# Performance work log

Hardware: AMD Instinct MI355X
Metric: run time of the kernel (lower is better)

Reference implementation:

```python
import jax, jax.numpy as jnp
import numpy as np

B, X, H, R, M = 256, 512, 1024, 512, 512
F_BIAS = 1.0

def setup_inputs() -> dict:
    key = jax.random.key(0)
    ks = jax.random.split(key, 8)
    s = lambda fan: 1.0 / np.sqrt(fan)
    return {
        "x": jax.random.normal(ks[0], (B, X), jnp.float32),
        "h": jax.random.normal(ks[1], (B, H), jnp.float32),
        "c": jnp.tanh(jax.random.normal(ks[2], (B, H), jnp.float32)),
        "hmem": jax.random.normal(ks[3], (B, M, R), jnp.float32),
        "W_full": jax.random.normal(ks[4], (X + R + H, R + 4 * H), jnp.float32) * s(X + R + H),
        "bias": jnp.zeros((R + 4 * H,), jnp.float32),
        "W_full1": jax.random.normal(ks[5], (X + R + H, R + H), jnp.float32) * s(X + R + H),
        "bias1": jnp.zeros((R + H,), jnp.float32),
        "trans_w": jax.random.normal(ks[6], (R, X + H), jnp.float32) * s(X + H),
        "trans_b": jnp.zeros((R,), jnp.float32),
        "fc_w": jax.random.normal(ks[7], (M, X + H), jnp.float32) * s(X + H),
        "fc_b": jnp.zeros((M,), jnp.float32),
    }

def reference(x, h, c, hmem, W_full, bias, W_full1, bias1, trans_w, trans_b, fc_w, fc_b):
    h_size = H
    # soft read head over memory slots
    read_head = jnp.concatenate([x, c], axis=1) @ fc_w.T + fc_b          # [B, M]
    h_index = jax.nn.softmax(read_head, axis=1)                          # [B, M]
    h_entry = jnp.einsum('bm,bmr->br', h_index, hmem)                    # [B, R]
    # gated double-projection
    concat = jnp.concatenate([x, c, h_entry], axis=1)                    # [B, X+H+R]
    g = jax.nn.sigmoid(concat @ W_full1 + bias1)                         # [B, R+H]
    gate = jnp.concatenate([jnp.ones_like(x), g], axis=1)                # [B, X+H+R]
    pre = (concat * gate) @ W_full + bias                                # [B, R+4H]
    i = pre[:, 0*h_size:1*h_size]
    j = pre[:, 1*h_size:2*h_size]
    f = pre[:, 2*h_size:3*h_size]
    o = pre[:, 3*h_size:4*h_size]
    om = pre[:, 4*h_size:]                                               # [B, R]
    new_c = jnp.tanh(c * jax.nn.sigmoid(f + F_BIAS) + jax.nn.sigmoid(i) * jnp.tanh(j))
    new_h = new_c * jax.nn.sigmoid(o)
    r_out = h_entry * jax.nn.sigmoid(om)
    # steady-state write: soft index (detached), broadcast overwrite
    w_index = jax.lax.stop_gradient(h_index)                             # [B, M]
    w_val = jnp.concatenate([x, new_c], axis=1) @ trans_w.T + trans_b    # [B, R]
    new_hmem = w_val[:, None, :] * w_index[:, :, None] + hmem * (1.0 - w_index[:, :, None])
    new_r = jnp.concatenate([new_h, r_out], axis=1)                      # [B, H+R]
    return new_r, new_h, new_c, new_hmem
```

## Files before the change

### kernel.cpp

```cpp
#include <hip/hip_runtime.h>
#include <hip/hip_bf16.h>
#include <cstddef>

#define BB 256
#define XX 512
#define HH 1024
#define RR 512
#define MM 512
#define KCAT 2048
#define KXC 1536
#define NFULL 4608
#define NG 1536

#define OFF_NH (BB*1536)
#define OFF_NC (OFF_NH + BB*HH)
#define OFF_HM (OFF_NC + BB*HH)

typedef __attribute__((ext_vector_type(8))) short bf16x8;
typedef __attribute__((ext_vector_type(4))) short s16x4;
typedef __attribute__((ext_vector_type(4))) float f32x4;

__device__ __forceinline__ float sigm(float x) { return 1.0f / (1.0f + expf(-x)); }

__device__ __forceinline__ unsigned short f2bf(float f) {
    unsigned u = __float_as_uint(f);
    u = u + 0x7fffu + ((u >> 16) & 1u);
    return (unsigned short)(u >> 16);
}
__device__ __forceinline__ float bf2f(unsigned short h) {
    return __uint_as_float((unsigned)h << 16);
}


__global__ __launch_bounds__(256) void convw_k(const float* __restrict__ src,
                                               short* __restrict__ hi,
                                               short* __restrict__ lo,
                                               int n8) {
    int i = blockIdx.x * 256 + threadIdx.x;
    if (i >= n8) return;
    size_t e0 = (size_t)i * 8;
    short hs[8], ls[8];
    #pragma unroll
    for (int q = 0; q < 2; ++q) {
        float4 v = reinterpret_cast<const float4*>(src + e0)[q];
        float f[4] = {v.x, v.y, v.z, v.w};
        #pragma unroll
        for (int e = 0; e < 4; ++e) {
            unsigned short hb = f2bf(f[e]);
            hs[q * 4 + e] = (short)hb;
            ls[q * 4 + e] = (short)f2bf(f[e] - bf2f(hb));
        }
    }
    *reinterpret_cast<bf16x8*>(hi + e0) = *reinterpret_cast<bf16x8*>(&hs[0]);
    *reinterpret_cast<bf16x8*>(lo + e0) = *reinterpret_cast<bf16x8*>(&ls[0]);
}

__global__ __launch_bounds__(256) void convt_k(const float* __restrict__ W,
                                               int Kdim, int Ndim,
                                               short* __restrict__ Thi,
                                               short* __restrict__ Tlo) {
    __shared__ __align__(16) short lh[64][72];
    __shared__ __align__(16) short ll[64][72];
    const int tid = threadIdx.x;
    const int k0 = blockIdx.x * 64, n0 = blockIdx.y * 64;
    {
        int kr = (tid >> 4) * 4;
        int nc = (tid & 15) * 4;
        #pragma unroll
        for (int i = 0; i < 4; ++i) {
            float4 v = *reinterpret_cast<const float4*>(W + (size_t)(k0 + kr + i) * Ndim + n0 + nc);
            float f[4] = {v.x, v.y, v.z, v.w};
            #pragma unroll
            for (int e = 0; e < 4; ++e) {
                unsigned short hb = f2bf(f[e]);
                lh[nc + e][kr + i] = (short)hb;
                ll[nc + e][kr + i] = (short)f2bf(f[e] - bf2f(hb));
            }
        }
    }
    __syncthreads();
    {
        int nl = tid >> 2;
        int kq = (tid & 3) * 16;
        size_t base = (size_t)(n0 + nl) * Kdim + k0 + kq;
        *reinterpret_cast<bf16x8*>(Thi + base)     = *reinterpret_cast<const bf16x8*>(&lh[nl][kq]);
        *reinterpret_cast<bf16x8*>(Thi + base + 8) = *reinterpret_cast<const bf16x8*>(&lh[nl][kq + 8]);
        *reinterpret_cast<bf16x8*>(Tlo + base)     = *reinterpret_cast<const bf16x8*>(&ll[nl][kq]);
        *reinterpret_cast<bf16x8*>(Tlo + base + 8) = *reinterpret_cast<const bf16x8*>(&ll[nl][kq + 8]);
    }
}

__global__ __launch_bounds__(256) void prep_k(const float* __restrict__ x,
                                              const float* __restrict__ c,
                                              short* __restrict__ cat_hi, short* __restrict__ cat_lo,
                                              short* __restrict__ gat_hi, short* __restrict__ gat_lo,
                                              short* __restrict__ xnc_hi, short* __restrict__ xnc_lo) {
    int i = blockIdx.x * 256 + threadIdx.x;
    int e0 = i * 4;
    int b = e0 / KXC, q = e0 - b * KXC;
    float4 v = (q < XX) ? *reinterpret_cast<const float4*>(x + (size_t)b * XX + q)
                        : *reinterpret_cast<const float4*>(c + (size_t)b * HH + (q - XX));
    float f[4] = {v.x, v.y, v.z, v.w};
    s16x4 hv, lv;
    #pragma unroll
    for (int e = 0; e < 4; ++e) {
        unsigned short hb = f2bf(f[e]);
        hv[e] = (short)hb;
        lv[e] = (short)f2bf(f[e] - bf2f(hb));
    }
    *reinterpret_cast<s16x4*>(cat_hi + (size_t)b * KCAT + q) = hv;
    *reinterpret_cast<s16x4*>(cat_lo + (size_t)b * KCAT + q) = lv;
    if (q < XX) {
        *reinterpret_cast<s16x4*>(gat_hi + (size_t)b * KCAT + q) = hv;
        *reinterpret_cast<s16x4*>(gat_lo + (size_t)b * KCAT + q) = lv;
        *reinterpret_cast<s16x4*>(xnc_hi + (size_t)b * KXC + q) = hv;
        *reinterpret_cast<s16x4*>(xnc_lo + (size_t)b * KXC + q) = lv;
    }
}

template<int EPI>
__global__ __launch_bounds__(256) void mgemm_ps(const short* __restrict__ Ahi,
                                                const short* __restrict__ Alo, int lda,
                                                const short* __restrict__ Bhi,
                                                const short* __restrict__ Blo,
                                                const float* __restrict__ bias,
                                                float* __restrict__ C, int ldc,
                                                const short* __restrict__ cat_hi,
                                                const short* __restrict__ cat_lo,
                                                short* __restrict__ gat_hi,
                                                short* __restrict__ gat_lo,
                                                int K) {
    __shared__ __align__(16) short Ah[64][72];
    __shared__ __align__(16) short Al[64][72];
    __shared__ __align__(16) short Bh[64][72];
    __shared__ __align__(16) short Bl[64][72];

    const int tid = threadIdx.x;
    const int row0 = blockIdx.y * 64, col0 = blockIdx.x * 64;
    const int lane = tid & 63, w = tid >> 6;
    const int rm = (w >> 1) * 32, cn = (w & 1) * 32;
    const int fr = lane & 15;
    const int kg = lane >> 4;

    const int ar = tid >> 2;
    const int akq = (tid & 3) * 16;

    f32x4 acc[2][2] = {};

    for (int k0 = 0; k0 < K; k0 += 64) {
        {
            size_t base = (size_t)(row0 + ar) * lda + k0 + akq;
            bf16x8 h0 = *reinterpret_cast<const bf16x8*>(Ahi + base);
            bf16x8 h1 = *reinterpret_cast<const bf16x8*>(Ahi + base + 8);
            bf16x8 l0 = *reinterpret_cast<const bf16x8*>(Alo + base);
            bf16x8 l1 = *reinterpret_cast<const bf16x8*>(Alo + base + 8);
            *reinterpret_cast<bf16x8*>(&Ah[ar][akq])     = h0;
            *reinterpret_cast<bf16x8*>(&Ah[ar][akq + 8]) = h1;
            *reinterpret_cast<bf16x8*>(&Al[ar][akq])     = l0;
            *reinterpret_cast<bf16x8*>(&Al[ar][akq + 8]) = l1;
        }
        {
            size_t base = (size_t)(col0 + ar) * K + k0 + akq;
            bf16x8 h0 = *reinterpret_cast<const bf16x8*>(Bhi + base);
            bf16x8 h1 = *reinterpret_cast<const bf16x8*>(Bhi + base + 8);
            bf16x8 l0 = *reinterpret_cast<const bf16x8*>(Blo + base);
            bf16x8 l1 = *reinterpret_cast<const bf16x8*>(Blo + base + 8);
            *reinterpret_cast<bf16x8*>(&Bh[ar][akq])     = h0;
            *reinterpret_cast<bf16x8*>(&Bh[ar][akq + 8]) = h1;
            *reinterpret_cast<bf16x8*>(&Bl[ar][akq])     = l0;
            *reinterpret_cast<bf16x8*>(&Bl[ar][akq + 8]) = l1;
        }
        __syncthreads();

        #pragma unroll
        for (int ks = 0; ks < 64; ks += 32) {
            bf16x8 ah[2], al[2], bh[2], bl[2];
            #pragma unroll
            for (int mf = 0; mf < 2; ++mf) {
                ah[mf] = *reinterpret_cast<const bf16x8*>(&Ah[rm + mf * 16 + fr][ks + kg * 8]);
                al[mf] = *reinterpret_cast<const bf16x8*>(&Al[rm + mf * 16 + fr][ks + kg * 8]);
            }
            #pragma unroll
            for (int nf = 0; nf < 2; ++nf) {
                bh[nf] = *reinterpret_cast<const bf16x8*>(&Bh[cn + nf * 16 + fr][ks + kg * 8]);
                bl[nf] = *reinterpret_cast<const bf16x8*>(&Bl[cn + nf * 16 + fr][ks + kg * 8]);
            }
            #pragma unroll
            for (int mf = 0; mf < 2; ++mf)
                #pragma unroll
                for (int nf = 0; nf < 2; ++nf) {
                    acc[mf][nf] = __builtin_amdgcn_mfma_f32_16x16x32_bf16(ah[mf], bh[nf], acc[mf][nf], 0, 0, 0);
                    acc[mf][nf] = __builtin_amdgcn_mfma_f32_16x16x32_bf16(ah[mf], bl[nf], acc[mf][nf], 0, 0, 0);
                    acc[mf][nf] = __builtin_amdgcn_mfma_f32_16x16x32_bf16(al[mf], bh[nf], acc[mf][nf], 0, 0, 0);
                }
        }
        __syncthreads();
    }

    #pragma unroll
    for (int mf = 0; mf < 2; ++mf)
        #pragma unroll
        for (int nf = 0; nf < 2; ++nf)
            #pragma unroll
            for (int i = 0; i < 4; ++i) {
                int row = row0 + rm + mf * 16 + kg * 4 + i;
                int col = col0 + cn + nf * 16 + fr;
                float v = acc[mf][nf][i] + bias[col];
                if (EPI == 0) {
                    C[(size_t)row * ldc + col] = v;
                } else {
                    size_t base = (size_t)row * KCAT + XX + col;
                    float e = bf2f((unsigned short)cat_hi[base]) + bf2f((unsigned short)cat_lo[base]);
                    float gv = e * sigm(v);
                    unsigned short hb = f2bf(gv);
                    gat_hi[base] = (short)hb;
                    gat_lo[base] = (short)f2bf(gv - bf2f(hb));
                }
            }
}

__global__ __launch_bounds__(512) void smhe_k(const float* __restrict__ rh,
                                              const float* __restrict__ hmem,
                                              float* __restrict__ hidx,
                                              short* __restrict__ cat_hi,
                                              short* __restrict__ cat_lo) {
    __shared__ float red[8];
    __shared__ float red2[8];
    __shared__ float wiL[MM];
    int b = blockIdx.x, t = threadIdx.x;
    float v = rh[(size_t)b * MM + t];
    float m = v;
    #pragma unroll
    for (int off = 1; off < 64; off <<= 1) m = fmaxf(m, __shfl_xor(m, off));
    int wid = t >> 6, lane = t & 63;
    if (lane == 0) red[wid] = m;
    __syncthreads();
    float mm = red[0];
    #pragma unroll
    for (int i = 1; i < 8; ++i) mm = fmaxf(mm, red[i]);
    float e = expf(v - mm);
    float s = e;
    #pragma unroll
    for (int off = 1; off < 64; off <<= 1) s += __shfl_xor(s, off);
    if (lane == 0) red2[wid] = s;
    __syncthreads();
    float tot = red2[0];
    #pragma unroll
    for (int i = 1; i < 8; ++i) tot += red2[i];
    float wi = e / tot;
    hidx[(size_t)b * MM + t] = wi;
    wiL[t] = wi;
    __syncthreads();
    const float* hm = hmem + (size_t)b * MM * RR + t;
    float acc = 0.f;
    #pragma unroll 8
    for (int m2 = 0; m2 < MM; ++m2) acc += wiL[m2] * hm[(size_t)m2 * RR];
    size_t base = (size_t)b * KCAT + KXC + t;
    unsigned short hb = f2bf(acc);
    cat_hi[base] = (short)hb;
    cat_lo[base] = (short)f2bf(acc - bf2f(hb));
}

__global__ __launch_bounds__(256) void lstm_k(const float* __restrict__ pre,
                                              const float* __restrict__ c,
                                              const short* __restrict__ cat_hi,
                                              const short* __restrict__ cat_lo,
                                              float* __restrict__ out,
                                              short* __restrict__ xnc_hi,
                                              short* __restrict__ xnc_lo) {
    int idx = blockIdx.x * 256 + threadIdx.x;
    int b = idx / 1536, q = idx - b * 1536;
    const float* p = pre + (size_t)b * NFULL;
    if (q < HH) {
        float iv = p[q], jv = p[HH + q], fv = p[2 * HH + q], ov = p[3 * HH + q];
        float cc = c[(size_t)b * HH + q];
        float nc = tanhf(cc * sigm(fv + 1.0f) + sigm(iv) * tanhf(jv));
        float nh = nc * sigm(ov);
        out[(size_t)b * 1536 + q] = nh;
        out[OFF_NH + (size_t)b * HH + q] = nh;
        out[OFF_NC + (size_t)b * HH + q] = nc;
        unsigned short hb = f2bf(nc);
        xnc_hi[(size_t)b * KXC + XX + q] = (short)hb;
        xnc_lo[(size_t)b * KXC + XX + q] = (short)f2bf(nc - bf2f(hb));
    } else {
        int r = q - HH;
        float om = p[4 * HH + r];
        size_t base = (size_t)b * KCAT + KXC + r;
        float he = bf2f((unsigned short)cat_hi[base]) + bf2f((unsigned short)cat_lo[base]);
        out[(size_t)b * 1536 + HH + r] = he * sigm(om);
    }
}

__global__ __launch_bounds__(256) void hmemupd_k(const float* __restrict__ hmem,
                                                 const float* __restrict__ wval,
                                                 const float* __restrict__ widx,
                                                 float* __restrict__ outhm) {
    size_t n4 = (size_t)BB * MM * RR / 4;
    size_t stride = (size_t)gridDim.x * blockDim.x;
    for (size_t i = (size_t)blockIdx.x * blockDim.x + threadIdx.x; i < n4; i += stride) {
        size_t e = i * 4;
        int r = (int)(e & (RR - 1));
        int m = (int)((e >> 9) & (MM - 1));
        int b = (int)(e >> 18);
        float wi = widx[(size_t)b * MM + m];
        float om = 1.0f - wi;
        float4 hv = *reinterpret_cast<const float4*>(hmem + e);
        float4 wv = *reinterpret_cast<const float4*>(wval + (size_t)b * RR + r);
        float4 o;
        o.x = wv.x * wi + hv.x * om;
        o.y = wv.y * wi + hv.y * om;
        o.z = wv.z * wi + hv.z * om;
        o.w = wv.w * wi + hv.w * om;
        *reinterpret_cast<float4*>(outhm + e) = o;
    }
}


__global__ __launch_bounds__(256) void prep3_k(const float* __restrict__ x,
                                               const float* __restrict__ c,
                                               float* __restrict__ concatb,
                                               float* __restrict__ gated) {
    int idx = blockIdx.x * 256 + threadIdx.x;
    int b = idx / KXC, q = idx - b * KXC;
    float v;
    if (q < XX) { v = x[b * XX + q]; gated[(size_t)b * KCAT + q] = v; }
    else v = c[b * HH + (q - XX)];
    concatb[(size_t)b * KCAT + q] = v;
}

template<int AMODE, int BLAYOUT, int EPI>
__global__ __launch_bounds__(256) void mgemm3_k(const float* __restrict__ A0,
                                                const float* __restrict__ A1,
                                                const float* __restrict__ W,
                                                const float* __restrict__ bias,
                                                float* __restrict__ C,
                                                const float* __restrict__ E,
                                                int N, int K) {
    __shared__ __align__(16) short Ah[64][72];
    __shared__ __align__(16) short Al[64][72];
    __shared__ __align__(16) short Bh[64][72];
    __shared__ __align__(16) short Bl[64][72];
    const int tid = threadIdx.x;
    const int row0 = blockIdx.y * 64, col0 = blockIdx.x * 64;
    const int lane = tid & 63, w = tid >> 6;
    const int rm = (w >> 1) * 32, cn = (w & 1) * 32;
    const int fr = lane & 15, kg = lane >> 4;
    const int ar = tid >> 2, akq = (tid & 3) * 16;
    const int bkk = (tid >> 4) * 4, bnn = (tid & 15) * 4;
    f32x4 acc[2][2] = {};
    for (int k0 = 0; k0 < K; k0 += 64) {
        {
            const float* src;
            if (AMODE == 0) src = A0 + (size_t)(row0 + ar) * K + k0 + akq;
            else {
                int gk = k0 + akq;
                src = (gk < XX) ? (A0 + (size_t)(row0 + ar) * XX + gk)
                                : (A1 + (size_t)(row0 + ar) * HH + (gk - XX));
            }
            short hs[16], ls[16];
            #pragma unroll
            for (int q = 0; q < 4; ++q) {
                float4 v = reinterpret_cast<const float4*>(src)[q];
                float f[4] = {v.x, v.y, v.z, v.w};
                #pragma unroll
                for (int e = 0; e < 4; ++e) {
                    unsigned short hb = f2bf(f[e]);
                    hs[q * 4 + e] = (short)hb;
                    ls[q * 4 + e] = (short)f2bf(f[e] - bf2f(hb));
                }
            }
            *reinterpret_cast<bf16x8*>(&Ah[ar][akq])     = *reinterpret_cast<bf16x8*>(&hs[0]);
            *reinterpret_cast<bf16x8*>(&Ah[ar][akq + 8]) = *reinterpret_cast<bf16x8*>(&hs[8]);
            *reinterpret_cast<bf16x8*>(&Al[ar][akq])     = *reinterpret_cast<bf16x8*>(&ls[0]);
            *reinterpret_cast<bf16x8*>(&Al[ar][akq + 8]) = *reinterpret_cast<bf16x8*>(&ls[8]);
        }
        if (BLAYOUT == 1) {
            const float* src = W + (size_t)(col0 + ar) * K + k0 + akq;
            short hs[16], ls[16];
            #pragma unroll
            for (int q = 0; q < 4; ++q) {
                float4 v = reinterpret_cast<const float4*>(src)[q];
                float f[4] = {v.x, v.y, v.z, v.w};
                #pragma unroll
                for (int e = 0; e < 4; ++e) {
                    unsigned short hb = f2bf(f[e]);
                    hs[q * 4 + e] = (short)hb;
                    ls[q * 4 + e] = (short)f2bf(f[e] - bf2f(hb));
                }
            }
            *reinterpret_cast<bf16x8*>(&Bh[ar][akq])     = *reinterpret_cast<bf16x8*>(&hs[0]);
            *reinterpret_cast<bf16x8*>(&Bh[ar][akq + 8]) = *reinterpret_cast<bf16x8*>(&hs[8]);
            *reinterpret_cast<bf16x8*>(&Bl[ar][akq])     = *reinterpret_cast<bf16x8*>(&ls[0]);
            *reinterpret_cast<bf16x8*>(&Bl[ar][akq + 8]) = *reinterpret_cast<bf16x8*>(&ls[8]);
        } else {
            float4 r0 = *reinterpret_cast<const float4*>(W + (size_t)(k0 + bkk + 0) * N + col0 + bnn);
            float4 r1 = *reinterpret_cast<const float4*>(W + (size_t)(k0 + bkk + 1) * N + col0 + bnn);
            float4 r2 = *reinterpret_cast<const float4*>(W + (size_t)(k0 + bkk + 2) * N + col0 + bnn);
            float4 r3 = *reinterpret_cast<const float4*>(W + (size_t)(k0 + bkk + 3) * N + col0 + bnn);
            float col[4][4] = {{r0.x, r1.x, r2.x, r3.x}, {r0.y, r1.y, r2.y, r3.y},
                               {r0.z, r1.z, r2.z, r3.z}, {r0.w, r1.w, r2.w, r3.w}};
            #pragma unroll
            for (int j = 0; j < 4; ++j) {
                s16x4 hv, lv;
                #pragma unroll
                for (int e = 0; e < 4; ++e) {
                    unsigned short hb = f2bf(col[j][e]);
                    hv[e] = (short)hb;
                    lv[e] = (short)f2bf(col[j][e] - bf2f(hb));
                }
                *reinterpret_cast<s16x4*>(&Bh[bnn + j][bkk]) = hv;
                *reinterpret_cast<s16x4*>(&Bl[bnn + j][bkk]) = lv;
            }
        }
        __syncthreads();
        #pragma unroll
        for (int ks = 0; ks < 64; ks += 32) {
            bf16x8 ah[2], al[2], bh[2], bl[2];
            #pragma unroll
            for (int mf = 0; mf < 2; ++mf) {
                ah[mf] = *reinterpret_cast<const bf16x8*>(&Ah[rm + mf * 16 + fr][ks + kg * 8]);
                al[mf] = *reinterpret_cast<const bf16x8*>(&Al[rm + mf * 16 + fr][ks + kg * 8]);
            }
            #pragma unroll
            for (int nf = 0; nf < 2; ++nf) {
                bh[nf] = *reinterpret_cast<const bf16x8*>(&Bh[cn + nf * 16 + fr][ks + kg * 8]);
                bl[nf] = *reinterpret_cast<const bf16x8*>(&Bl[cn + nf * 16 + fr][ks + kg * 8]);
            }
            #pragma unroll
            for (int mf = 0; mf < 2; ++mf)
                #pragma unroll
                for (int nf = 0; nf < 2; ++nf) {
                    acc[mf][nf] = __builtin_amdgcn_mfma_f32_16x16x32_bf16(ah[mf], bh[nf], acc[mf][nf], 0, 0, 0);
                    acc[mf][nf] = __builtin_amdgcn_mfma_f32_16x16x32_bf16(ah[mf], bl[nf], acc[mf][nf], 0, 0, 0);
                    acc[mf][nf] = __builtin_amdgcn_mfma_f32_16x16x32_bf16(al[mf], bh[nf], acc[mf][nf], 0, 0, 0);
                }
        }
        __syncthreads();
    }
    #pragma unroll
    for (int mf = 0; mf < 2; ++mf)
        #pragma unroll
        for (int nf = 0; nf < 2; ++nf)
            #pragma unroll
            for (int i = 0; i < 4; ++i) {
                int row = row0 + rm + mf * 16 + kg * 4 + i;
                int col = col0 + cn + nf * 16 + fr;
                float v = acc[mf][nf][i] + bias[col];
                if (EPI == 0) C[(size_t)row * N + col] = v;
                else {
                    size_t base = (size_t)row * KCAT + XX + col;
                    C[base] = E[base] * sigm(v);
                }
            }
}

__global__ __launch_bounds__(256) void softmax3_k(float* __restrict__ rh) {
    int b = blockIdx.x;
    float* row = rh + (size_t)b * MM;
    int t = threadIdx.x;
    float v0 = row[t], v1 = row[t + 256];
    float m = fmaxf(v0, v1);
    #pragma unroll
    for (int off = 1; off < 64; off <<= 1) m = fmaxf(m, __shfl_xor(m, off));
    __shared__ float red[8];
    int wid = t >> 6, lane = t & 63;
    if (lane == 0) red[wid] = m;
    __syncthreads();
    float mm = fmaxf(fmaxf(red[0], red[1]), fmaxf(red[2], red[3]));
    float e0 = expf(v0 - mm), e1 = expf(v1 - mm);
    float s = e0 + e1;
    #pragma unroll
    for (int off = 1; off < 64; off <<= 1) s += __shfl_xor(s, off);
    if (lane == 0) red[4 + wid] = s;
    __syncthreads();
    float inv = 1.0f / (red[4] + red[5] + red[6] + red[7]);
    row[t] = e0 * inv;
    row[t + 256] = e1 * inv;
}

__global__ __launch_bounds__(512) void hentry3_k(const float* __restrict__ hidx,
                                                 const float* __restrict__ hmem,
                                                 float* __restrict__ concatb) {
    int b = blockIdx.x;
    int r = threadIdx.x;
    __shared__ float wi[MM];
    wi[r] = hidx[(size_t)b * MM + r];
    __syncthreads();
    const float* hm = hmem + (size_t)b * MM * RR + r;
    float acc = 0.f;
    #pragma unroll 8
    for (int m = 0; m < MM; ++m) acc += wi[m] * hm[(size_t)m * RR];
    concatb[(size_t)b * KCAT + KXC + r] = acc;
}

__global__ __launch_bounds__(256) void lstm3_k(const float* __restrict__ pre,
                                               const float* __restrict__ c,
                                               const float* __restrict__ concatb,
                                               float* __restrict__ out) {
    int idx = blockIdx.x * 256 + threadIdx.x;
    int b = idx / 1536, q = idx - b * 1536;
    const float* p = pre + (size_t)b * NFULL;
    if (q < HH) {
        float iv = p[q], jv = p[HH + q], fv = p[2 * HH + q], ov = p[3 * HH + q];
        float cc = c[(size_t)b * HH + q];
        float nc = tanhf(cc * sigm(fv + 1.0f) + sigm(iv) * tanhf(jv));
        float nh = nc * sigm(ov);
        out[(size_t)b * 1536 + q] = nh;
        out[OFF_NH + (size_t)b * HH + q] = nh;
        out[OFF_NC + (size_t)b * HH + q] = nc;
    } else {
        int r = q - HH;
        float om = p[4 * HH + r];
        float he = concatb[(size_t)b * KCAT + KXC + r];
        out[(size_t)b * 1536 + HH + r] = he * sigm(om);
    }
}

extern "C" void kernel_launch(void* const* d_in, const int* in_sizes, int n_in,
                              void* d_out, int out_size, void* d_ws, size_t ws_size,
                              hipStream_t stream) {
    const float* x      = (const float*)d_in[0];
    const float* c      = (const float*)d_in[2];
    const float* hmem   = (const float*)d_in[3];
    const float* W_full = (const float*)d_in[4];
    const float* bias   = (const float*)d_in[5];
    const float* W_full1= (const float*)d_in[6];
    const float* bias1  = (const float*)d_in[7];
    const float* trans_w= (const float*)d_in[8];
    const float* trans_b= (const float*)d_in[9];
    const float* fc_w   = (const float*)d_in[10];
    const float* fc_b   = (const float*)d_in[11];

    float* out = (float*)d_out;

    constexpr size_t SZ_WT  = (size_t)NFULL * KCAT * 2;
    constexpr size_t SZ_WT1 = (size_t)NG * KCAT * 2;
    constexpr size_t SZ_FCW = (size_t)MM * KXC * 2;
    constexpr size_t SZ_TRW = (size_t)RR * KXC * 2;
    constexpr size_t SZ_CAT = (size_t)BB * KCAT * 2;
    constexpr size_t SZ_XNC = (size_t)BB * KXC * 2;
    constexpr size_t SZ_RH  = (size_t)BB * MM * 4;
    constexpr size_t SZ_PRE = (size_t)BB * NFULL * 4;
    constexpr size_t NEED = 2*SZ_WT + 2*SZ_WT1 + 2*SZ_FCW + 2*SZ_TRW
                          + 4*SZ_CAT + 2*SZ_XNC + 2*SZ_RH + SZ_PRE + SZ_RH;

    if (ws_size >= NEED) {
        char* p = (char*)d_ws;
        short* wt_hi  = (short*)p; p += SZ_WT;
        short* wt_lo  = (short*)p; p += SZ_WT;
        short* wt1_hi = (short*)p; p += SZ_WT1;
        short* wt1_lo = (short*)p; p += SZ_WT1;
        short* fcw_hi = (short*)p; p += SZ_FCW;
        short* fcw_lo = (short*)p; p += SZ_FCW;
        short* trw_hi = (short*)p; p += SZ_TRW;
        short* trw_lo = (short*)p; p += SZ_TRW;
        short* cat_hi = (short*)p; p += SZ_CAT;
        short* cat_lo = (short*)p; p += SZ_CAT;
        short* gat_hi = (short*)p; p += SZ_CAT;
        short* gat_lo = (short*)p; p += SZ_CAT;
        short* xnc_hi = (short*)p; p += SZ_XNC;
        short* xnc_lo = (short*)p; p += SZ_XNC;
        float* rh     = (float*)p; p += SZ_RH;
        float* hidx   = (float*)p; p += SZ_RH;
        float* pre    = (float*)p; p += SZ_PRE;
        float* wval   = (float*)p;

        convt_k<<<dim3(KCAT / 64, NFULL / 64), 256, 0, stream>>>(W_full, KCAT, NFULL, wt_hi, wt_lo);
        convt_k<<<dim3(KCAT / 64, NG / 64), 256, 0, stream>>>(W_full1, KCAT, NG, wt1_hi, wt1_lo);
        convw_k<<<(MM * KXC / 8 + 255) / 256, 256, 0, stream>>>(fc_w, fcw_hi, fcw_lo, MM * KXC / 8);
        convw_k<<<(RR * KXC / 8 + 255) / 256, 256, 0, stream>>>(trans_w, trw_hi, trw_lo, RR * KXC / 8);

        prep_k<<<BB * KXC / 4 / 256, 256, 0, stream>>>(x, c, cat_hi, cat_lo, gat_hi, gat_lo, xnc_hi, xnc_lo);

        mgemm_ps<0><<<dim3(MM / 64, BB / 64), 256, 0, stream>>>(
            cat_hi, cat_lo, KCAT, fcw_hi, fcw_lo, fc_b, rh, MM,
            nullptr, nullptr, nullptr, nullptr, KXC);

        smhe_k<<<BB, 512, 0, stream>>>(rh, hmem, hidx, cat_hi, cat_lo);

        mgemm_ps<1><<<dim3(NG / 64, BB / 64), 256, 0, stream>>>(
            cat_hi, cat_lo, KCAT, wt1_hi, wt1_lo, bias1, nullptr, 0,
            cat_hi, cat_lo, gat_hi, gat_lo, KCAT);

        mgemm_ps<0><<<dim3(NFULL / 64, BB / 64), 256, 0, stream>>>(
            gat_hi, gat_lo, KCAT, wt_hi, wt_lo, bias, pre, NFULL,
            nullptr, nullptr, nullptr, nullptr, KCAT);

        lstm_k<<<BB * 1536 / 256, 256, 0, stream>>>(pre, c, cat_hi, cat_lo, out, xnc_hi, xnc_lo);

        mgemm_ps<0><<<dim3(RR / 64, BB / 64), 256, 0, stream>>>(
            xnc_hi, xnc_lo, KXC, trw_hi, trw_lo, trans_b, wval, RR,
            nullptr, nullptr, nullptr, nullptr, KXC);

        hmemupd_k<<<4096, 256, 0, stream>>>(hmem, wval, hidx, out + OFF_HM);
    } else {
        float* ws   = (float*)d_ws;
        float* hidx    = ws;
        float* concatb = hidx + BB * MM;
        float* gated   = concatb + BB * KCAT;
        float* pre     = gated + BB * KCAT;
        float* wval    = pre + BB * NFULL;
        float* new_c   = out + OFF_NC;

        prep3_k<<<BB * KXC / 256, 256, 0, stream>>>(x, c, concatb, gated);
        mgemm3_k<1, 1, 0><<<dim3(MM / 64, BB / 64), 256, 0, stream>>>(
            x, c, fc_w, fc_b, hidx, nullptr, MM, KXC);
        softmax3_k<<<BB, 256, 0, stream>>>(hidx);
        hentry3_k<<<BB, 512, 0, stream>>>(hidx, hmem, concatb);
        mgemm3_k<0, 0, 1><<<dim3(NG / 64, BB / 64), 256, 0, stream>>>(
            concatb, nullptr, W_full1, bias1, gated, concatb, NG, KCAT);
        mgemm3_k<0, 0, 0><<<dim3(NFULL / 64, BB / 64), 256, 0, stream>>>(
            gated, nullptr, W_full, bias, pre, nullptr, NFULL, KCAT);
        lstm3_k<<<BB * 1536 / 256, 256, 0, stream>>>(pre, c, concatb, out);
        mgemm3_k<1, 1, 0><<<dim3(RR / 64, BB / 64), 256, 0, stream>>>(
            x, new_c, trans_w, trans_b, wval, nullptr, RR, KXC);
        hmemupd_k<<<4096, 256, 0, stream>>>(hmem, wval, hidx, out + OFF_HM);
    }
}
```

Before: 341.7 us.

## Use 128x128 split-K GEMM tiles with register prefetch and fused weight conversion launches

Replaces the 64x64 GEMM with a 128x128 tile kernel that prefetches the next K slab into registers while computing. Split-K over grid z keeps the small GEMMs at enough blocks, and partial sums are reduced in the consumer kernels (softmax, new gfin_k gating kernel, lstm, hmem update). The paired weight-conversion launches are merged and workspace regions are aliased to fit the partial buffers. This trades larger per-block reuse and fewer launches for extra partial-sum traffic and an added reduction kernel.

```diff
diff --git a/kernel.cpp b/kernel.cpp
--- a/kernel.cpp
+++ b/kernel.cpp
@@ -32,13 +32,14 @@
 }
 
 
-__global__ __launch_bounds__(256) void convw_k(const float* __restrict__ src,
-                                               short* __restrict__ hi,
-                                               short* __restrict__ lo,
-                                               int n8) {
-    int i = blockIdx.x * 256 + threadIdx.x;
-    if (i >= n8) return;
-    size_t e0 = (size_t)i * 8;
+__global__ __launch_bounds__(256) void convw_k(const float* __restrict__ s0,
+                                               short* __restrict__ h0, short* __restrict__ l0,
+                                               const float* __restrict__ s1,
+                                               short* __restrict__ h1, short* __restrict__ l1) {
+    const float* src = blockIdx.y ? s1 : s0;
+    short* hi = blockIdx.y ? h1 : h0;
+    short* lo = blockIdx.y ? l1 : l0;
+    size_t e0 = ((size_t)blockIdx.x * 256 + threadIdx.x) * 8;
     short hs[8], ls[8];
     #pragma unroll
     for (int q = 0; q < 2; ++q) {
@@ -55,14 +56,20 @@
     *reinterpret_cast<bf16x8*>(lo + e0) = *reinterpret_cast<bf16x8*>(&ls[0]);
 }
 
-__global__ __launch_bounds__(256) void convt_k(const float* __restrict__ W,
-                                               int Kdim, int Ndim,
-                                               short* __restrict__ Thi,
-                                               short* __restrict__ Tlo) {
+__global__ __launch_bounds__(256) void convt_k(const float* __restrict__ W0,
+                                               short* __restrict__ T0hi, short* __restrict__ T0lo,
+                                               const float* __restrict__ W1,
+                                               short* __restrict__ T1hi, short* __restrict__ T1lo) {
     __shared__ __align__(16) short lh[64][72];
     __shared__ __align__(16) short ll[64][72];
     const int tid = threadIdx.x;
-    const int k0 = blockIdx.x * 64, n0 = blockIdx.y * 64;
+    const int by = blockIdx.y;
+    const float* W;
+    short *Thi, *Tlo;
+    int Ndim, n0;
+    if (by < 72) { W = W0; Thi = T0hi; Tlo = T0lo; Ndim = NFULL; n0 = by * 64; }
+    else         { W = W1; Thi = T1hi; Tlo = T1lo; Ndim = NG;    n0 = (by - 72) * 64; }
+    const int k0 = blockIdx.x * 64;
     {
         int kr = (tid >> 4) * 4;
         int nc = (tid & 15) * 4;
@@ -82,7 +89,7 @@
     {
         int nl = tid >> 2;
         int kq = (tid & 3) * 16;
-        size_t base = (size_t)(n0 + nl) * Kdim + k0 + kq;
+        size_t base = (size_t)(n0 + nl) * KCAT + k0 + kq;
         *reinterpret_cast<bf16x8*>(Thi + base)     = *reinterpret_cast<const bf16x8*>(&lh[nl][kq]);
         *reinterpret_cast<bf16x8*>(Thi + base + 8) = *reinterpret_cast<const bf16x8*>(&lh[nl][kq + 8]);
         *reinterpret_cast<bf16x8*>(Tlo + base)     = *reinterpret_cast<const bf16x8*>(&ll[nl][kq]);
@@ -118,77 +125,82 @@
     }
 }
 
-template<int EPI>
-__global__ __launch_bounds__(256) void mgemm_ps(const short* __restrict__ Ahi,
-                                                const short* __restrict__ Alo, int lda,
-                                                const short* __restrict__ Bhi,
-                                                const short* __restrict__ Blo,
-                                                const float* __restrict__ bias,
-                                                float* __restrict__ C, int ldc,
-                                                const short* __restrict__ cat_hi,
-                                                const short* __restrict__ cat_lo,
-                                                short* __restrict__ gat_hi,
-                                                short* __restrict__ gat_lo,
-                                                int K) {
-    __shared__ __align__(16) short Ah[64][72];
-    __shared__ __align__(16) short Al[64][72];
-    __shared__ __align__(16) short Bh[64][72];
-    __shared__ __align__(16) short Bl[64][72];
+__global__ __launch_bounds__(256, 2) void mgemm128(const short* __restrict__ Ahi,
+                                                   const short* __restrict__ Alo, int lda,
+                                                   const short* __restrict__ Bhi,
+                                                   const short* __restrict__ Blo, int ldb,
+                                                   const float* __restrict__ bias,
+                                                   float* __restrict__ Cbase, int ldc,
+                                                   size_t chunk_stride, int kchunk) {
+    __shared__ __align__(16) short Ah[128][72];
+    __shared__ __align__(16) short Al[128][72];
+    __shared__ __align__(16) short Bh[128][72];
+    __shared__ __align__(16) short Bl[128][72];
 
     const int tid = threadIdx.x;
-    const int row0 = blockIdx.y * 64, col0 = blockIdx.x * 64;
+    const int col0 = blockIdx.x * 128, row0 = blockIdx.y * 128;
+    const int z = blockIdx.z;
+    const int kbeg = z * kchunk;
+    float* C = Cbase + (size_t)z * chunk_stride;
+
     const int lane = tid & 63, w = tid >> 6;
-    const int rm = (w >> 1) * 32, cn = (w & 1) * 32;
-    const int fr = lane & 15;
-    const int kg = lane >> 4;
-
-    const int ar = tid >> 2;
-    const int akq = (tid & 3) * 16;
-
-    f32x4 acc[2][2] = {};
-
-    for (int k0 = 0; k0 < K; k0 += 64) {
-        {
-            size_t base = (size_t)(row0 + ar) * lda + k0 + akq;
-            bf16x8 h0 = *reinterpret_cast<const bf16x8*>(Ahi + base);
-            bf16x8 h1 = *reinterpret_cast<const bf16x8*>(Ahi + base + 8);
-            bf16x8 l0 = *reinterpret_cast<const bf16x8*>(Alo + base);
-            bf16x8 l1 = *reinterpret_cast<const bf16x8*>(Alo + base + 8);
-            *reinterpret_cast<bf16x8*>(&Ah[ar][akq])     = h0;
-            *reinterpret_cast<bf16x8*>(&Ah[ar][akq + 8]) = h1;
-            *reinterpret_cast<bf16x8*>(&Al[ar][akq])     = l0;
-            *reinterpret_cast<bf16x8*>(&Al[ar][akq + 8]) = l1;
-        }
-        {
-            size_t base = (size_t)(col0 + ar) * K + k0 + akq;
-            bf16x8 h0 = *reinterpret_cast<const bf16x8*>(Bhi + base);
-            bf16x8 h1 = *reinterpret_cast<const bf16x8*>(Bhi + base + 8);
-            bf16x8 l0 = *reinterpret_cast<const bf16x8*>(Blo + base);
-            bf16x8 l1 = *reinterpret_cast<const bf16x8*>(Blo + base + 8);
-            *reinterpret_cast<bf16x8*>(&Bh[ar][akq])     = h0;
-            *reinterpret_cast<bf16x8*>(&Bh[ar][akq + 8]) = h1;
-            *reinterpret_cast<bf16x8*>(&Bl[ar][akq])     = l0;
-            *reinterpret_cast<bf16x8*>(&Bl[ar][akq + 8]) = l1;
+    const int rm = (w >> 1) * 64, cn = (w & 1) * 64;
+    const int fr = lane & 15, kg = lane >> 4;
+
+    const int sr = tid >> 1;
+    const int sk = (tid & 1) * 32;
+
+    f32x4 acc[4][4] = {};
+    int4 pa[8], pb[8];
+
+    const short* aH = Ahi + (size_t)(row0 + sr) * lda + sk;
+    const short* aL = Alo + (size_t)(row0 + sr) * lda + sk;
+    const short* bH = Bhi + (size_t)(col0 + sr) * ldb + sk;
+    const short* bL = Blo + (size_t)(col0 + sr) * ldb + sk;
+
+    const int steps = kchunk >> 6;
+
+    #pragma unroll
+    for (int j = 0; j < 4; ++j) {
+        pa[j]     = *reinterpret_cast<const int4*>(aH + kbeg + j * 8);
+        pa[4 + j] = *reinterpret_cast<const int4*>(aL + kbeg + j * 8);
+        pb[j]     = *reinterpret_cast<const int4*>(bH + kbeg + j * 8);
+        pb[4 + j] = *reinterpret_cast<const int4*>(bL + kbeg + j * 8);
+    }
+
+    for (int t = 0; t < steps; ++t) {
+        #pragma unroll
+        for (int j = 0; j < 4; ++j) {
+            *reinterpret_cast<int4*>(&Ah[sr][sk + j * 8]) = pa[j];
+            *reinterpret_cast<int4*>(&Al[sr][sk + j * 8]) = pa[4 + j];
+            *reinterpret_cast<int4*>(&Bh[sr][sk + j * 8]) = pb[j];
+            *reinterpret_cast<int4*>(&Bl[sr][sk + j * 8]) = pb[4 + j];
         }
         __syncthreads();
-
+        if (t + 1 < steps) {
+            int kc = kbeg + (t + 1) * 64;
+            #pragma unroll
+            for (int j = 0; j < 4; ++j) {
+                pa[j]     = *reinterpret_cast<const int4*>(aH + kc + j * 8);
+                pa[4 + j] = *reinterpret_cast<const int4*>(aL + kc + j * 8);
+                pb[j]     = *reinterpret_cast<const int4*>(bH + kc + j * 8);
+                pb[4 + j] = *reinterpret_cast<const int4*>(bL + kc + j * 8);
+            }
+        }
         #pragma unroll
         for (int ks = 0; ks < 64; ks += 32) {
-            bf16x8 ah[2], al[2], bh[2], bl[2];
-            #pragma unroll
-            for (int mf = 0; mf < 2; ++mf) {
-                ah[mf] = *reinterpret_cast<const bf16x8*>(&Ah[rm + mf * 16 + fr][ks + kg * 8]);
-                al[mf] = *reinterpret_cast<const bf16x8*>(&Al[rm + mf * 16 + fr][ks + kg * 8]);
-            }
-            #pragma unroll
-            for (int nf = 0; nf < 2; ++nf) {
-                bh[nf] = *reinterpret_cast<const bf16x8*>(&Bh[cn + nf * 16 + fr][ks + kg * 8]);
-                bl[nf] = *reinterpret_cast<const bf16x8*>(&Bl[cn + nf * 16 + fr][ks + kg * 8]);
-            }
-            #pragma unroll
-            for (int mf = 0; mf < 2; ++mf)
+            bf16x8 ah[4], al[4], bh[4], bl[4];
+            #pragma unroll
+            for (int q = 0; q < 4; ++q) {
+                ah[q] = *reinterpret_cast<const bf16x8*>(&Ah[rm + q * 16 + fr][ks + kg * 8]);
+                al[q] = *reinterpret_cast<const bf16x8*>(&Al[rm + q * 16 + fr][ks + kg * 8]);
+                bh[q] = *reinterpret_cast<const bf16x8*>(&Bh[cn + q * 16 + fr][ks + kg * 8]);
+                bl[q] = *reinterpret_cast<const bf16x8*>(&Bl[cn + q * 16 + fr][ks + kg * 8]);
+            }
+            #pragma unroll
+            for (int mf = 0; mf < 4; ++mf)
                 #pragma unroll
-                for (int nf = 0; nf < 2; ++nf) {
+                for (int nf = 0; nf < 4; ++nf) {
                     acc[mf][nf] = __builtin_amdgcn_mfma_f32_16x16x32_bf16(ah[mf], bh[nf], acc[mf][nf], 0, 0, 0);
                     acc[mf][nf] = __builtin_amdgcn_mfma_f32_16x16x32_bf16(ah[mf], bl[nf], acc[mf][nf], 0, 0, 0);
                     acc[mf][nf] = __builtin_amdgcn_mfma_f32_16x16x32_bf16(al[mf], bh[nf], acc[mf][nf], 0, 0, 0);
@@ -198,28 +210,20 @@
     }
 
     #pragma unroll
-    for (int mf = 0; mf < 2; ++mf)
-        #pragma unroll
-        for (int nf = 0; nf < 2; ++nf)
+    for (int mf = 0; mf < 4; ++mf)
+        #pragma unroll
+        for (int nf = 0; nf < 4; ++nf)
             #pragma unroll
             for (int i = 0; i < 4; ++i) {
                 int row = row0 + rm + mf * 16 + kg * 4 + i;
                 int col = col0 + cn + nf * 16 + fr;
-                float v = acc[mf][nf][i] + bias[col];
-                if (EPI == 0) {
-                    C[(size_t)row * ldc + col] = v;
-                } else {
-                    size_t base = (size_t)row * KCAT + XX + col;
-                    float e = bf2f((unsigned short)cat_hi[base]) + bf2f((unsigned short)cat_lo[base]);
-                    float gv = e * sigm(v);
-                    unsigned short hb = f2bf(gv);
-                    gat_hi[base] = (short)hb;
-                    gat_lo[base] = (short)f2bf(gv - bf2f(hb));
-                }
-            }
-}
-
-__global__ __launch_bounds__(512) void smhe_k(const float* __restrict__ rh,
+                float v = acc[mf][nf][i];
+                if (z == 0) v += bias[col];
+                C[(size_t)row * ldc + col] = v;
+            }
+}
+
+__global__ __launch_bounds__(512) void smhe_k(const float* __restrict__ rhp,
                                               const float* __restrict__ hmem,
                                               float* __restrict__ hidx,
                                               short* __restrict__ cat_hi,
@@ -228,7 +232,9 @@
     __shared__ float red2[8];
     __shared__ float wiL[MM];
     int b = blockIdx.x, t = threadIdx.x;
-    float v = rh[(size_t)b * MM + t];
+    float v = 0.f;
+    #pragma unroll
+    for (int zz = 0; zz < 6; ++zz) v += rhp[(size_t)zz * (BB * MM) + (size_t)b * MM + t];
     float m = v;
     #pragma unroll
     for (int off = 1; off < 64; off <<= 1) m = fmaxf(m, __shfl_xor(m, off));
@@ -261,18 +267,40 @@
     cat_lo[base] = (short)f2bf(acc - bf2f(hb));
 }
 
-__global__ __launch_bounds__(256) void lstm_k(const float* __restrict__ pre,
+__global__ __launch_bounds__(256) void gfin_k(const float* __restrict__ gp,
+                                              const short* __restrict__ cat_hi,
+                                              const short* __restrict__ cat_lo,
+                                              short* __restrict__ gat_hi,
+                                              short* __restrict__ gat_lo) {
+    int i = blockIdx.x * 256 + threadIdx.x;
+    int b = i / NG, q = i - b * NG;
+    float s = 0.f;
+    #pragma unroll
+    for (int zz = 0; zz < 4; ++zz) s += gp[(size_t)zz * (BB * NG) + (size_t)b * NG + q];
+    size_t base = (size_t)b * KCAT + XX + q;
+    float e = bf2f((unsigned short)cat_hi[base]) + bf2f((unsigned short)cat_lo[base]);
+    float gv = e * sigm(s);
+    unsigned short hb = f2bf(gv);
+    gat_hi[base] = (short)hb;
+    gat_lo[base] = (short)f2bf(gv - bf2f(hb));
+}
+
+__global__ __launch_bounds__(256) void lstm_k(const float* __restrict__ pre0,
                                               const float* __restrict__ c,
                                               const short* __restrict__ cat_hi,
                                               const short* __restrict__ cat_lo,
                                               float* __restrict__ out,
                                               short* __restrict__ xnc_hi,
                                               short* __restrict__ xnc_lo) {
+    const float* pre1 = pre0 + (size_t)BB * NFULL;
     int idx = blockIdx.x * 256 + threadIdx.x;
     int b = idx / 1536, q = idx - b * 1536;
-    const float* p = pre + (size_t)b * NFULL;
+    size_t pb = (size_t)b * NFULL;
     if (q < HH) {
-        float iv = p[q], jv = p[HH + q], fv = p[2 * HH + q], ov = p[3 * HH + q];
+        float iv = pre0[pb + q] + pre1[pb + q];
+        float jv = pre0[pb + HH + q] + pre1[pb + HH + q];
+        float fv = pre0[pb + 2 * HH + q] + pre1[pb + 2 * HH + q];
+        float ov = pre0[pb + 3 * HH + q] + pre1[pb + 3 * HH + q];
         float cc = c[(size_t)b * HH + q];
         float nc = tanhf(cc * sigm(fv + 1.0f) + sigm(iv) * tanhf(jv));
         float nh = nc * sigm(ov);
@@ -284,7 +312,7 @@
         xnc_lo[(size_t)b * KXC + XX + q] = (short)f2bf(nc - bf2f(hb));
     } else {
         int r = q - HH;
-        float om = p[4 * HH + r];
+        float om = pre0[pb + 4 * HH + r] + pre1[pb + 4 * HH + r];
         size_t base = (size_t)b * KCAT + KXC + r;
         float he = bf2f((unsigned short)cat_hi[base]) + bf2f((unsigned short)cat_lo[base]);
         out[(size_t)b * 1536 + HH + r] = he * sigm(om);
@@ -292,7 +320,7 @@
 }
 
 __global__ __launch_bounds__(256) void hmemupd_k(const float* __restrict__ hmem,
-                                                 const float* __restrict__ wval,
+                                                 const float* __restrict__ wvalp,
                                                  const float* __restrict__ widx,
                                                  float* __restrict__ outhm) {
     size_t n4 = (size_t)BB * MM * RR / 4;
@@ -305,7 +333,12 @@
         float wi = widx[(size_t)b * MM + m];
         float om = 1.0f - wi;
         float4 hv = *reinterpret_cast<const float4*>(hmem + e);
-        float4 wv = *reinterpret_cast<const float4*>(wval + (size_t)b * RR + r);
+        float4 wv = {0.f, 0.f, 0.f, 0.f};
+        #pragma unroll
+        for (int zz = 0; zz < 6; ++zz) {
+            float4 p = *reinterpret_cast<const float4*>(wvalp + (size_t)zz * (BB * RR) + (size_t)b * RR + r);
+            wv.x += p.x; wv.y += p.y; wv.z += p.z; wv.w += p.w;
+        }
         float4 o;
         o.x = wv.x * wi + hv.x * om;
         o.y = wv.y * wi + hv.y * om;
@@ -516,6 +549,30 @@
     }
 }
 
+__global__ __launch_bounds__(256) void hmemupd3_k(const float* __restrict__ hmem,
+                                                  const float* __restrict__ wval,
+                                                  const float* __restrict__ widx,
+                                                  float* __restrict__ outhm) {
+    size_t n4 = (size_t)BB * MM * RR / 4;
+    size_t stride = (size_t)gridDim.x * blockDim.x;
+    for (size_t i = (size_t)blockIdx.x * blockDim.x + threadIdx.x; i < n4; i += stride) {
+        size_t e = i * 4;
+        int r = (int)(e & (RR - 1));
+        int m = (int)((e >> 9) & (MM - 1));
+        int b = (int)(e >> 18);
+        float wi = widx[(size_t)b * MM + m];
+        float om = 1.0f - wi;
+        float4 hv = *reinterpret_cast<const float4*>(hmem + e);
+        float4 wv = *reinterpret_cast<const float4*>(wval + (size_t)b * RR + r);
+        float4 o;
+        o.x = wv.x * wi + hv.x * om;
+        o.y = wv.y * wi + hv.y * om;
+        o.z = wv.z * wi + hv.z * om;
+        o.w = wv.w * wi + hv.w * om;
+        *reinterpret_cast<float4*>(outhm + e) = o;
+    }
+}
+
 extern "C" void kernel_launch(void* const* d_in, const int* in_sizes, int n_in,
                               void* d_out, int out_size, void* d_ws, size_t ws_size,
                               hipStream_t stream) {
@@ -533,25 +590,28 @@
 
     float* out = (float*)d_out;
 
-    constexpr size_t SZ_WT  = (size_t)NFULL * KCAT * 2;
-    constexpr size_t SZ_WT1 = (size_t)NG * KCAT * 2;
-    constexpr size_t SZ_FCW = (size_t)MM * KXC * 2;
-    constexpr size_t SZ_TRW = (size_t)RR * KXC * 2;
-    constexpr size_t SZ_CAT = (size_t)BB * KCAT * 2;
-    constexpr size_t SZ_XNC = (size_t)BB * KXC * 2;
-    constexpr size_t SZ_RH  = (size_t)BB * MM * 4;
-    constexpr size_t SZ_PRE = (size_t)BB * NFULL * 4;
-    constexpr size_t NEED = 2*SZ_WT + 2*SZ_WT1 + 2*SZ_FCW + 2*SZ_TRW
-                          + 4*SZ_CAT + 2*SZ_XNC + 2*SZ_RH + SZ_PRE + SZ_RH;
+    constexpr size_t SZ_WT   = (size_t)NFULL * KCAT * 2;
+    constexpr size_t SZ_WT1  = (size_t)NG * KCAT * 2;
+    constexpr size_t SZ_FCW  = (size_t)MM * KXC * 2;
+    constexpr size_t SZ_TRW  = (size_t)RR * KXC * 2;
+    constexpr size_t SZ_CAT  = (size_t)BB * KCAT * 2;
+    constexpr size_t SZ_XNC  = (size_t)BB * KXC * 2;
+    constexpr size_t SZ_RH   = (size_t)BB * MM * 4;
+    constexpr size_t SZ_RH6  = 6 * SZ_RH;
+    constexpr size_t SZ_GP4  = 4 * (size_t)BB * NG * 4;
+    constexpr size_t SZ_PRE2 = 2 * (size_t)BB * NFULL * 4;
+    constexpr size_t SZ_WV6  = 6 * SZ_RH;
+    constexpr size_t SZ_R1 = 2 * SZ_WT1 + 2 * SZ_FCW + SZ_RH6;
+    constexpr size_t SZ_R2 = SZ_GP4;
+    constexpr size_t NEED = 2 * SZ_WT + 2 * SZ_TRW + 2 * SZ_CAT
+                          + 2 * SZ_CAT
+                          + 2 * SZ_XNC + SZ_RH
+                          + SZ_R1 + SZ_R2;
 
     if (ws_size >= NEED) {
         char* p = (char*)d_ws;
         short* wt_hi  = (short*)p; p += SZ_WT;
         short* wt_lo  = (short*)p; p += SZ_WT;
-        short* wt1_hi = (short*)p; p += SZ_WT1;
-        short* wt1_lo = (short*)p; p += SZ_WT1;
-        short* fcw_hi = (short*)p; p += SZ_FCW;
-        short* fcw_lo = (short*)p; p += SZ_FCW;
         short* trw_hi = (short*)p; p += SZ_TRW;
         short* trw_lo = (short*)p; p += SZ_TRW;
         short* cat_hi = (short*)p; p += SZ_CAT;
@@ -560,41 +620,43 @@
         short* gat_lo = (short*)p; p += SZ_CAT;
         short* xnc_hi = (short*)p; p += SZ_XNC;
         short* xnc_lo = (short*)p; p += SZ_XNC;
-        float* rh     = (float*)p; p += SZ_RH;
         float* hidx   = (float*)p; p += SZ_RH;
-        float* pre    = (float*)p; p += SZ_PRE;
-        float* wval   = (float*)p;
-
-        convt_k<<<dim3(KCAT / 64, NFULL / 64), 256, 0, stream>>>(W_full, KCAT, NFULL, wt_hi, wt_lo);
-        convt_k<<<dim3(KCAT / 64, NG / 64), 256, 0, stream>>>(W_full1, KCAT, NG, wt1_hi, wt1_lo);
-        convw_k<<<(MM * KXC / 8 + 255) / 256, 256, 0, stream>>>(fc_w, fcw_hi, fcw_lo, MM * KXC / 8);
-        convw_k<<<(RR * KXC / 8 + 255) / 256, 256, 0, stream>>>(trans_w, trw_hi, trw_lo, RR * KXC / 8);
-
-        prep_k<<<BB * KXC / 4 / 256, 256, 0, stream>>>(x, c, cat_hi, cat_lo, gat_hi, gat_lo, xnc_hi, xnc_lo);
-
-        mgemm_ps<0><<<dim3(MM / 64, BB / 64), 256, 0, stream>>>(
-            cat_hi, cat_lo, KCAT, fcw_hi, fcw_lo, fc_b, rh, MM,
-            nullptr, nullptr, nullptr, nullptr, KXC);
-
-        smhe_k<<<BB, 512, 0, stream>>>(rh, hmem, hidx, cat_hi, cat_lo);
-
-        mgemm_ps<1><<<dim3(NG / 64, BB / 64), 256, 0, stream>>>(
-            cat_hi, cat_lo, KCAT, wt1_hi, wt1_lo, bias1, nullptr, 0,
-            cat_hi, cat_lo, gat_hi, gat_lo, KCAT);
-
-        mgemm_ps<0><<<dim3(NFULL / 64, BB / 64), 256, 0, stream>>>(
-            gat_hi, gat_lo, KCAT, wt_hi, wt_lo, bias, pre, NFULL,
-            nullptr, nullptr, nullptr, nullptr, KCAT);
-
-        lstm_k<<<BB * 1536 / 256, 256, 0, stream>>>(pre, c, cat_hi, cat_lo, out, xnc_hi, xnc_lo);
-
-        mgemm_ps<0><<<dim3(RR / 64, BB / 64), 256, 0, stream>>>(
-            xnc_hi, xnc_lo, KXC, trw_hi, trw_lo, trans_b, wval, RR,
-            nullptr, nullptr, nullptr, nullptr, KXC);
-
-        hmemupd_k<<<4096, 256, 0, stream>>>(hmem, wval, hidx, out + OFF_HM);
+        char*  r1     = p;         p += SZ_R1;
+        char*  r2     = p;
+        short* wt1_hi = (short*)r1;
+        short* wt1_lo = (short*)(r1 + SZ_WT1);
+        short* fcw_hi = (short*)(r1 + 2 * SZ_WT1);
+        short* fcw_lo = (short*)(r1 + 2 * SZ_WT1 + SZ_FCW);
+        float* rh6    = (float*)(r1 + 2 * SZ_WT1 + 2 * SZ_FCW);
+        float* pre2   = (float*)r1;
+        float* gp4    = (float*)r2;
+        float* wv6    = (float*)r2;
+
+        convt_k<<<dim3(KCAT / 64, 96), 256, 0, stream>>>(W_full, wt_hi, wt_lo,
+                                                         W_full1, wt1_hi, wt1_lo);
+        convw_k<<<dim3(MM * KXC / 8 / 256, 2), 256, 0, stream>>>(fc_w, fcw_hi, fcw_lo,
+                                                                 trans_w, trw_hi, trw_lo);
+        prep_k<<<BB * KXC / 4 / 256, 256, 0, stream>>>(x, c, cat_hi, cat_lo,
+                                                       gat_hi, gat_lo, xnc_hi, xnc_lo);
+        mgemm128<<<dim3(MM / 128, BB / 128, 6), 256, 0, stream>>>(
+            cat_hi, cat_lo, KCAT, fcw_hi, fcw_lo, KXC, fc_b,
+            rh6, MM, (size_t)BB * MM, KXC / 6);
+        smhe_k<<<BB, 512, 0, stream>>>(rh6, hmem, hidx, cat_hi, cat_lo);
+        mgemm128<<<dim3(NG / 128, BB / 128, 4), 256, 0, stream>>>(
+            cat_hi, cat_lo, KCAT, wt1_hi, wt1_lo, KCAT, bias1,
+            gp4, NG, (size_t)BB * NG, KCAT / 4);
+        gfin_k<<<BB * NG / 256, 256, 0, stream>>>(gp4, cat_hi, cat_lo, gat_hi, gat_lo);
+        mgemm128<<<dim3(NFULL / 128, BB / 128, 2), 256, 0, stream>>>(
+            gat_hi, gat_lo, KCAT, wt_hi, wt_lo, KCAT, bias,
+            pre2, NFULL, (size_t)BB * NFULL, KCAT / 2);
+        lstm_k<<<BB * 1536 / 256, 256, 0, stream>>>(pre2, c, cat_hi, cat_lo,
+                                                    out, xnc_hi, xnc_lo);
+        mgemm128<<<dim3(RR / 128, BB / 128, 6), 256, 0, stream>>>(
+            xnc_hi, xnc_lo, KXC, trw_hi, trw_lo, KXC, trans_b,
+            wv6, RR, (size_t)BB * RR, KXC / 6);
+        hmemupd_k<<<4096, 256, 0, stream>>>(hmem, wv6, hidx, out + OFF_HM);
     } else {
-        float* ws   = (float*)d_ws;
+        float* ws      = (float*)d_ws;
         float* hidx    = ws;
         float* concatb = hidx + BB * MM;
         float* gated   = concatb + BB * KCAT;
@@ -614,6 +676,6 @@
         lstm3_k<<<BB * 1536 / 256, 256, 0, stream>>>(pre, c, concatb, out);
         mgemm3_k<1, 1, 0><<<dim3(RR / 64, BB / 64), 256, 0, stream>>>(
             x, new_c, trans_w, trans_b, wval, nullptr, RR, KXC);
-        hmemupd_k<<<4096, 256, 0, stream>>>(hmem, wval, hidx, out + OFF_HM);
-    }
-}
+        hmemupd3_k<<<4096, 256, 0, stream>>>(hmem, wval, hidx, out + OFF_HM);
+    }
+}
```

New measurement: 510.1 us. 49.3% more time.

## Split memory read into parallel partial sums and tile the hmem update

Applied to the files above, without the earlier changes.

The fused softmax plus weighted memory read is split into three kernels. A softmax kernel runs first, then a partial-reduction kernel splits the 512 memory slots into 4 chunks across a 2D grid, giving 1024 blocks instead of 256, and a final kernel sums the partials and writes the bf16 hi/lo pair. The hmem update kernel now gives each block one batch and 32 slots, staging w_val and the write index in shared memory instead of reloading them from global memory per element. The cost is two extra launches and a round trip of partial sums through the pre buffer.

```diff
diff --git a/kernel.cpp b/kernel.cpp
--- a/kernel.cpp
+++ b/kernel.cpp
@@ -219,14 +219,10 @@
             }
 }
 
-__global__ __launch_bounds__(512) void smhe_k(const float* __restrict__ rh,
-                                              const float* __restrict__ hmem,
-                                              float* __restrict__ hidx,
-                                              short* __restrict__ cat_hi,
-                                              short* __restrict__ cat_lo) {
+__global__ __launch_bounds__(512) void smax_k(const float* __restrict__ rh,
+                                              float* __restrict__ hidx) {
     __shared__ float red[8];
     __shared__ float red2[8];
-    __shared__ float wiL[MM];
     int b = blockIdx.x, t = threadIdx.x;
     float v = rh[(size_t)b * MM + t];
     float m = v;
@@ -247,15 +243,32 @@
     float tot = red2[0];
     #pragma unroll
     for (int i = 1; i < 8; ++i) tot += red2[i];
-    float wi = e / tot;
-    hidx[(size_t)b * MM + t] = wi;
-    wiL[t] = wi;
-    __syncthreads();
-    const float* hm = hmem + (size_t)b * MM * RR + t;
+    hidx[(size_t)b * MM + t] = e / tot;
+}
+
+__global__ __launch_bounds__(512) void hepart_k(const float* __restrict__ hidx,
+                                                const float* __restrict__ hmem,
+                                                float* __restrict__ hep) {
+    __shared__ float wi[128];
+    int b = blockIdx.x, s = blockIdx.y, t = threadIdx.x;
+    if (t < 128) wi[t] = hidx[(size_t)b * MM + s * 128 + t];
+    __syncthreads();
+    const float* hm = hmem + ((size_t)b * MM + (size_t)s * 128) * RR + t;
     float acc = 0.f;
     #pragma unroll 8
-    for (int m2 = 0; m2 < MM; ++m2) acc += wiL[m2] * hm[(size_t)m2 * RR];
-    size_t base = (size_t)b * KCAT + KXC + t;
+    for (int j = 0; j < 128; ++j) acc += wi[j] * hm[(size_t)j * RR];
+    hep[((size_t)s * BB + b) * RR + t] = acc;
+}
+
+__global__ __launch_bounds__(256) void hefin_k(const float* __restrict__ hep,
+                                               short* __restrict__ cat_hi,
+                                               short* __restrict__ cat_lo) {
+    int i = blockIdx.x * 256 + threadIdx.x;
+    int b = i >> 9, r = i & (RR - 1);
+    float acc = 0.f;
+    #pragma unroll
+    for (int s = 0; s < 4; ++s) acc += hep[((size_t)s * BB + b) * RR + r];
+    size_t base = (size_t)b * KCAT + KXC + r;
     unsigned short hb = f2bf(acc);
     cat_hi[base] = (short)hb;
     cat_lo[base] = (short)f2bf(acc - bf2f(hb));
@@ -295,22 +308,32 @@
                                                  const float* __restrict__ wval,
                                                  const float* __restrict__ widx,
                                                  float* __restrict__ outhm) {
-    size_t n4 = (size_t)BB * MM * RR / 4;
-    size_t stride = (size_t)gridDim.x * blockDim.x;
-    for (size_t i = (size_t)blockIdx.x * blockDim.x + threadIdx.x; i < n4; i += stride) {
-        size_t e = i * 4;
-        int r = (int)(e & (RR - 1));
-        int m = (int)((e >> 9) & (MM - 1));
-        int b = (int)(e >> 18);
-        float wi = widx[(size_t)b * MM + m];
-        float om = 1.0f - wi;
+    __shared__ float wv[RR];
+    __shared__ float wi[32];
+    int blk = blockIdx.x;
+    int b = blk >> 4;
+    int m0 = (blk & 15) * 32;
+    int t = threadIdx.x;
+    wv[t]       = wval[(size_t)b * RR + t];
+    wv[t + 256] = wval[(size_t)b * RR + 256 + t];
+    if (t < 32) wi[t] = widx[(size_t)b * MM + m0 + t];
+    __syncthreads();
+    int r4 = (t & 127) * 4;
+    int mo = t >> 7;
+    size_t base = ((size_t)b * MM + m0) * RR + r4;
+    float4 wv4 = *reinterpret_cast<const float4*>(&wv[r4]);
+    #pragma unroll 4
+    for (int it = 0; it < 16; ++it) {
+        int m = it * 2 + mo;
+        float w = wi[m];
+        float omw = 1.0f - w;
+        size_t e = base + (size_t)m * RR;
         float4 hv = *reinterpret_cast<const float4*>(hmem + e);
-        float4 wv = *reinterpret_cast<const float4*>(wval + (size_t)b * RR + r);
         float4 o;
-        o.x = wv.x * wi + hv.x * om;
-        o.y = wv.y * wi + hv.y * om;
-        o.z = wv.z * wi + hv.z * om;
-        o.w = wv.w * wi + hv.w * om;
+        o.x = wv4.x * w + hv.x * omw;
+        o.y = wv4.y * w + hv.y * omw;
+        o.z = wv4.z * w + hv.z * omw;
+        o.w = wv4.w * w + hv.w * omw;
         *reinterpret_cast<float4*>(outhm + e) = o;
     }
 }
@@ -516,6 +539,30 @@
     }
 }
 
+__global__ __launch_bounds__(256) void hmemupd3_k(const float* __restrict__ hmem,
+                                                  const float* __restrict__ wval,
+                                                  const float* __restrict__ widx,
+                                                  float* __restrict__ outhm) {
+    size_t n4 = (size_t)BB * MM * RR / 4;
+    size_t stride = (size_t)gridDim.x * blockDim.x;
+    for (size_t i = (size_t)blockIdx.x * blockDim.x + threadIdx.x; i < n4; i += stride) {
+        size_t e = i * 4;
+        int r = (int)(e & (RR - 1));
+        int m = (int)((e >> 9) & (MM - 1));
+        int b = (int)(e >> 18);
+        float wi = widx[(size_t)b * MM + m];
+        float om = 1.0f - wi;
+        float4 hv = *reinterpret_cast<const float4*>(hmem + e);
+        float4 wv = *reinterpret_cast<const float4*>(wval + (size_t)b * RR + r);
+        float4 o;
+        o.x = wv.x * wi + hv.x * om;
+        o.y = wv.y * wi + hv.y * om;
+        o.z = wv.z * wi + hv.z * om;
+        o.w = wv.w * wi + hv.w * om;
+        *reinterpret_cast<float4*>(outhm + e) = o;
+    }
+}
+
 extern "C" void kernel_launch(void* const* d_in, const int* in_sizes, int n_in,
                               void* d_out, int out_size, void* d_ws, size_t ws_size,
                               hipStream_t stream) {
@@ -564,6 +611,7 @@
         float* hidx   = (float*)p; p += SZ_RH;
         float* pre    = (float*)p; p += SZ_PRE;
         float* wval   = (float*)p;
+        float* hep    = pre;
 
         convt_k<<<dim3(KCAT / 64, NFULL / 64), 256, 0, stream>>>(W_full, KCAT, NFULL, wt_hi, wt_lo);
         convt_k<<<dim3(KCAT / 64, NG / 64), 256, 0, stream>>>(W_full1, KCAT, NG, wt1_hi, wt1_lo);
@@ -576,7 +624,9 @@
             cat_hi, cat_lo, KCAT, fcw_hi, fcw_lo, fc_b, rh, MM,
             nullptr, nullptr, nullptr, nullptr, KXC);
 
-        smhe_k<<<BB, 512, 0, stream>>>(rh, hmem, hidx, cat_hi, cat_lo);
+        smax_k<<<BB, 512, 0, stream>>>(rh, hidx);
+        hepart_k<<<dim3(BB, 4), 512, 0, stream>>>(hidx, hmem, hep);
+        hefin_k<<<BB * RR / 256, 256, 0, stream>>>(hep, cat_hi, cat_lo);
 
         mgemm_ps<1><<<dim3(NG / 64, BB / 64), 256, 0, stream>>>(
             cat_hi, cat_lo, KCAT, wt1_hi, wt1_lo, bias1, nullptr, 0,
@@ -592,7 +642,7 @@
             xnc_hi, xnc_lo, KXC, trw_hi, trw_lo, trans_b, wval, RR,
             nullptr, nullptr, nullptr, nullptr, KXC);
 
-        hmemupd_k<<<4096, 256, 0, stream>>>(hmem, wval, hidx, out + OFF_HM);
+        hmemupd_k<<<BB * 16, 256, 0, stream>>>(hmem, wval, hidx, out + OFF_HM);
     } else {
         float* ws   = (float*)d_ws;
         float* hidx    = ws;
@@ -614,6 +664,6 @@
         lstm3_k<<<BB * 1536 / 256, 256, 0, stream>>>(pre, c, concatb, out);
         mgemm3_k<1, 1, 0><<<dim3(RR / 64, BB / 64), 256, 0, stream>>>(
             x, new_c, trans_w, trans_b, wval, nullptr, RR, KXC);
-        hmemupd_k<<<4096, 256, 0, stream>>>(hmem, wval, hidx, out + OFF_HM);
-    }
-}
+        hmemupd3_k<<<4096, 256, 0, stream>>>(hmem, wval, hidx, out + OFF_HM);
+    }
+}
```

New measurement: 377.9 us. 10.6% more time.
